# Optimization experiments

Measured on AMD Instinct MI355X. Metric: run time of the kernel, lower is better.

Reference implementation:

```python
import jax, jax.numpy as jnp
import numpy as np

B, T, D, H = 4, 3072, 1024, 16
HD = D // H

def setup_inputs() -> dict:
    key = jax.random.key(0)
    ks = jax.random.split(key, 7)
    s = 1.0 / np.sqrt(D)
    x = jax.random.normal(ks[0], (B, T, D), dtype=jnp.float32)
    Wq = jax.random.normal(ks[1], (D, D), dtype=jnp.float32) * s
    Wk = jax.random.normal(ks[2], (D, D), dtype=jnp.float32) * s
    Wv = jax.random.normal(ks[3], (D, D), dtype=jnp.float32) * s
    Wo = jax.random.normal(ks[4], (D, D), dtype=jnp.float32) * s
    bo = jnp.zeros((D,), dtype=jnp.float32)
    Wconv = jax.random.normal(ks[5], (D, D, 3), dtype=jnp.float32) * (1.0 / np.sqrt(3 * D))  # (out, in, kw)
    return {"x": x, "Wq": Wq, "Wk": Wk, "Wv": Wv, "Wo": Wo, "bo": bo, "Wconv": Wconv}

def reference(x, Wq, Wk, Wv, Wo, bo, Wconv):
    b, t, d = x.shape
    # stride-3 conv pooling of K/V stream (Conv1d(D, D, 3, stride=3, bias=False))
    kc = jax.lax.conv_general_dilated(
        x.transpose(0, 2, 1), Wconv, window_strides=(3,), padding='VALID',
        dimension_numbers=('NCH', 'OIH', 'NCH')).transpose(0, 2, 1)  # (B, T//3, D)
    k_tmp = jnp.concatenate([x[:, :1, :], kc], axis=1)  # (B, Tk, D)
    tk = k_tmp.shape[1]
    # comparison-based bias mask: masked where 3*k_idx >= q_idx + 0.001
    q_idx = jnp.arange(t, dtype=jnp.float32)
    k_idx = jnp.arange(tk, dtype=jnp.float32)
    mask = (k_idx[None, :] * 3.0 >= q_idx[:, None] + 0.001).astype(x.dtype)  # (T, Tk)
    # projections (torch Linear: y = x @ W.T)
    q = x @ Wq.T
    k = k_tmp @ Wk.T
    v = k_tmp @ Wv.T
    q = q.reshape(b, t, H, HD).transpose(0, 2, 1, 3)   # (B, H, T, HD)
    k = k.reshape(b, tk, H, HD).transpose(0, 2, 1, 3)  # (B, H, Tk, HD)
    v = v.reshape(b, tk, H, HD).transpose(0, 2, 1, 3)
    scores = jnp.einsum('bhqd,bhkd->bhqk', q, k) * (HD ** -0.5)
    scores = scores + mask * jnp.asarray(-1e9, dtype=x.dtype)
    p = jax.nn.softmax(scores, axis=-1)  # dropout is identity in eval (p=0)
    o = jnp.einsum('bhqk,bhkd->bhqd', p, v)
    o = o.transpose(0, 2, 1, 3).reshape(b, t, d)
    return o @ Wo.T + bo
```

## Files before the change

### kernel.cpp

```cpp
#include <hip/hip_runtime.h>
#include <hip/hip_bf16.h>
#include <cstdint>
#include <cstddef>

typedef __attribute__((ext_vector_type(8))) __bf16 bf16x8;
typedef __attribute__((ext_vector_type(4))) __bf16 bf16x4;
typedef __attribute__((ext_vector_type(4))) float  floatx4;

#define MFMA16x16x32(a, b, c) __builtin_amdgcn_mfma_f32_16x16x32_bf16((a), (b), (c), 0, 0, 0)

#define ATTN_SC 0.18033688011112042f

__device__ __forceinline__ void gload_lds16(const void* g, void* l) {
  __builtin_amdgcn_global_load_lds((const __attribute__((address_space(1))) void*)g,
                                   (__attribute__((address_space(3))) void*)l,
                                   16, 0, 0);
}


__global__ void prep_kernel(const float* __restrict__ x,
                            const float* __restrict__ Wq, const float* __restrict__ Wk,
                            const float* __restrict__ Wv, const float* __restrict__ Wo,
                            const float* __restrict__ Wconv,
                            __bf16* __restrict__ xb,
                            __bf16* __restrict__ wqb, __bf16* __restrict__ wkb,
                            __bf16* __restrict__ wvb, __bf16* __restrict__ wob,
                            __bf16* __restrict__ wc2, __bf16* __restrict__ ktmp) {
  const int bid = blockIdx.x, tid = threadIdx.x;
  if (bid < 4096) {
    const int which = bid >> 10;
    const float* src = (which == 0) ? Wq : (which == 1) ? Wk : (which == 2) ? Wv : Wo;
    __bf16* dst = (which == 0) ? wqb : (which == 1) ? wkb : (which == 2) ? wvb : wob;
    const int i = (bid & 1023) * 256 + tid;
    floatx4 v = *(const floatx4*)(src + (size_t)i * 4);
    bf16x4 o; o[0] = (__bf16)v[0]; o[1] = (__bf16)v[1]; o[2] = (__bf16)v[2]; o[3] = (__bf16)v[3];
    *(bf16x4*)(dst + (size_t)i * 4) = o;
  } else if (bid < 5120) {
    const int t = (bid - 4096) * 256 + tid;
    const int o = t >> 8, c = t & 255;
    const float* base = Wconv + (size_t)o * 3072 + c * 12;
    float f[12];
    *(floatx4*)(f)     = *(const floatx4*)(base);
    *(floatx4*)(f + 4) = *(const floatx4*)(base + 4);
    *(floatx4*)(f + 8) = *(const floatx4*)(base + 8);
#pragma unroll
    for (int kw = 0; kw < 3; ++kw) {
      bf16x4 q;
#pragma unroll
      for (int j = 0; j < 4; ++j) q[j] = (__bf16)f[3 * j + kw];
      *(bf16x4*)(wc2 + (size_t)o * 3072 + kw * 1024 + c * 4) = q;
    }
  } else if (bid < 5136) {
    const int i = (bid - 5120) * 256 + tid;
    const int b = i >> 10, c = i & 1023;
    ktmp[(size_t)b * 1025 * 1024 + c] = (__bf16)x[(size_t)b * 3072 * 1024 + c];
  } else {
    const int i = (bid - 5136) * 256 + tid;
    floatx4 v = *(const floatx4*)(x + (size_t)i * 4);
    bf16x4 o; o[0] = (__bf16)v[0]; o[1] = (__bf16)v[1]; o[2] = (__bf16)v[2]; o[3] = (__bf16)v[3];
    *(bf16x4*)(xb + (size_t)i * 4) = o;
  }
}

__global__ void vtrans_kernel(const __bf16* __restrict__ V, __bf16* __restrict__ Vt) {
  __shared__ __attribute__((aligned(16))) __bf16 tile[64][72];
  const int tid = threadIdx.x;
  const int bh = blockIdx.y;
  const int b = bh >> 4, h = bh & 15;
  const int t0 = blockIdx.x * 64;
  const int r = tid >> 3, s = tid & 7;
#pragma unroll
  for (int p = 0; p < 2; ++p) {
    const int t = p * 32 + r;
    bf16x8 v = *(const bf16x8*)(V + ((size_t)(b * 1025 + t0 + t)) * 1024 + h * 64 + s * 8);
    *(bf16x8*)(&tile[t][s * 8]) = v;
  }
  __syncthreads();
#pragma unroll
  for (int p = 0; p < 2; ++p) {
    const int d = p * 32 + r;
    bf16x8 o;
#pragma unroll
    for (int e = 0; e < 8; ++e) o[e] = tile[s * 8 + e][d];
    *(bf16x8*)(Vt + ((size_t)bh * 64 + d) * 1024 + t0 + s * 8) = o;
  }
}


template <int MODE>
__device__ __forceinline__ void gemm8_body(
    const __bf16* __restrict__ A, const __bf16* __restrict__ Bw, void* __restrict__ Cout,
    const float* __restrict__ bias, int N, int K, int m0, int n0,
    __bf16* As, __bf16* Bs)
{
  const int tid  = threadIdx.x;
  const int wave = tid >> 6;
  const int lane = tid & 63;
  const int g    = lane >> 4;
  const int ln   = lane & 15;
  const int wr   = (wave >> 2) * 64;
  const int wc   = (wave & 3) * 64;

  const int prow = tid >> 3;
  const int pc   = tid & 7;
  const int ca   = pc ^ (prow & 7);
  const size_t aSrc  = (size_t)(m0 + prow + ((ca >> 2) << 6)) * K + ((ca & 3) << 3);
  const size_t bSrc0 = (size_t)(n0 + prow + ((ca >> 2) << 7)) * K + ((ca & 3) << 3);
  const size_t bSrc1 = bSrc0 + (size_t)64 * K;

  int aOff[4], bOff[4];
#pragma unroll
  for (int i = 0; i < 4; ++i) {
    const int ra = wr + i * 16 + ln;
    const int pr = ra & 63;
    const int c  = ((ra >> 6) << 2) + g;
    aOff[i] = pr * 64 + ((c ^ (pr & 7)) << 3);
  }
#pragma unroll
  for (int j = 0; j < 4; ++j) {
    const int rb = wc + j * 16 + ln;
    const int pr = rb & 127;
    const int c  = ((rb >> 7) << 2) + g;
    bOff[j] = pr * 64 + ((c ^ (pr & 7)) << 3);
  }

  floatx4 acc[4][4];
#pragma unroll
  for (int i = 0; i < 4; ++i)
#pragma unroll
    for (int j = 0; j < 4; ++j) { floatx4 z = {0.f, 0.f, 0.f, 0.f}; acc[i][j] = z; }

  __bf16* const ad0 = As + (tid << 3);
  __bf16* const bd0 = Bs + (tid << 3);

  auto STAGE = [&](int halfidx) {
    const int slot = halfidx & 3;
    const int koff = (halfidx >> 1) * 64 + ((halfidx & 1) << 5);
    gload_lds16(A  + aSrc  + koff, ad0 + (slot << 12));
    gload_lds16(Bw + bSrc0 + koff, bd0 + (slot << 13));
    gload_lds16(Bw + bSrc1 + koff, bd0 + (slot << 13) + 4096);
  };

  bf16x8 afA[4], bfA[4], afB[4], bfB[4];

#define READF(AF, BF, slot)                                                        \
  {                                                                                \
    const __bf16* ah_ = As + ((slot) << 12);                                       \
    const __bf16* bh_ = Bs + ((slot) << 13);                                       \
    _Pragma("unroll")                                                              \
    for (int i_ = 0; i_ < 4; ++i_) AF[i_] = *(const bf16x8*)(ah_ + aOff[i_]);      \
    _Pragma("unroll")                                                              \
    for (int j_ = 0; j_ < 4; ++j_) BF[j_] = *(const bf16x8*)(bh_ + bOff[j_]);      \
  }

#define MFMAC(AF, BF)                                                              \
  {                                                                                \
    __builtin_amdgcn_s_setprio(1);                                                 \
    _Pragma("unroll")                                                              \
    for (int i_ = 0; i_ < 4; ++i_)                                                 \
      _Pragma("unroll")                                                            \
      for (int j_ = 0; j_ < 4; ++j_)                                               \
        acc[i_][j_] = MFMA16x16x32(AF[i_], BF[j_], acc[i_][j_]);                   \
    __builtin_amdgcn_s_setprio(0);                                                 \
  }

#define PHASE_WAIT(x)                                                              \
  {                                                                                \
    if ((x) + 4 < HT)      { asm volatile("s_waitcnt vmcnt(6) lgkmcnt(0)" ::: "memory"); } \
    else if ((x) + 3 < HT) { asm volatile("s_waitcnt vmcnt(3) lgkmcnt(0)" ::: "memory"); } \
    else                   { asm volatile("s_waitcnt vmcnt(0) lgkmcnt(0)" ::: "memory"); } \
  }

  const int HT = K >> 5;

  STAGE(0); STAGE(1); STAGE(2);
  asm volatile("s_waitcnt vmcnt(6)" ::: "memory");
  __builtin_amdgcn_s_barrier();
  __builtin_amdgcn_sched_barrier(0);
  READF(afA, bfA, 0);
  STAGE(3);
  asm volatile("s_waitcnt vmcnt(6) lgkmcnt(0)" ::: "memory");

  for (int h = 0; h < HT; h += 2) {
    __builtin_amdgcn_s_barrier();
    __builtin_amdgcn_sched_barrier(0);
    READF(afB, bfB, (h + 1) & 3);
    MFMAC(afA, bfA);
    if (h + 4 < HT) STAGE(h + 4);
    PHASE_WAIT(h);

    __builtin_amdgcn_s_barrier();
    __builtin_amdgcn_sched_barrier(0);
    if (h + 2 < HT) READF(afA, bfA, (h + 2) & 3);
    MFMAC(afB, bfB);
    if (h + 2 < HT) {
      if (h + 5 < HT) STAGE(h + 5);
      PHASE_WAIT(h + 1);
    }
  }

#undef READF
#undef MFMAC
#undef PHASE_WAIT

#pragma unroll
  for (int j = 0; j < 4; ++j) {
    const int col = n0 + wc + j * 16 + ln;
    float bj = 0.f;
    if (MODE == 2) bj = bias[col];
#pragma unroll
    for (int i = 0; i < 4; ++i)
#pragma unroll
      for (int r = 0; r < 4; ++r) {
        const int row = m0 + wr + i * 16 + g * 4 + r;
        if (MODE == 2) {
          ((float*)Cout)[(size_t)row * N + col] = acc[i][j][r] + bj;
        } else if (MODE == 1) {
          const size_t orow = (size_t)(row >> 10) * 1025 + 1 + (row & 1023);
          ((__bf16*)Cout)[orow * 1024 + col] = (__bf16)acc[i][j][r];
        } else if (MODE == 4) {
          ((__bf16*)Cout)[(size_t)row * N + col] = (__bf16)(acc[i][j][r] * ATTN_SC);
        } else {
          ((__bf16*)Cout)[(size_t)row * N + col] = (__bf16)acc[i][j][r];
        }
      }
  }
}

__global__ __launch_bounds__(512, 2) void gemm_convq_kernel(
    const __bf16* __restrict__ xb, const __bf16* __restrict__ wc2,
    const __bf16* __restrict__ wqb, __bf16* __restrict__ ktmp, __bf16* __restrict__ qb)
{
  __shared__ __attribute__((aligned(16))) __bf16 As[16384];
  __shared__ __attribute__((aligned(16))) __bf16 Bs[32768];
  const int xcd = blockIdx.x & 7, s = blockIdx.x >> 3;
  if (s < 16) {
    const int id = xcd * 16 + s;
    gemm8_body<1>(xb, wc2, ktmp, nullptr, 1024, 3072, (id >> 2) * 128, (id & 3) * 256, As, Bs);
  } else {
    const int id = xcd * 48 + (s - 16);
    gemm8_body<4>(xb, wqb, qb, nullptr, 1024, 1024, (id >> 2) * 128, (id & 3) * 256, As, Bs);
  }
}

__global__ __launch_bounds__(512, 2) void gemm_kv_kernel(
    const __bf16* __restrict__ ktmp, const __bf16* __restrict__ wkb,
    const __bf16* __restrict__ wvb, __bf16* __restrict__ kb, __bf16* __restrict__ vb)
{
  __shared__ __attribute__((aligned(16))) __bf16 As[16384];
  __shared__ __attribute__((aligned(16))) __bf16 Bs[32768];
  const int id = (blockIdx.x & 7) * 33 + (blockIdx.x >> 3);
  const int p  = (id >= 132) ? 1 : 0;
  const int rest = id - p * 132;
  gemm8_body<0>(ktmp, p ? wvb : wkb, p ? vb : kb, nullptr, 1024, 1024,
                (rest >> 2) * 128, (rest & 3) * 256, As, Bs);
}

__global__ __launch_bounds__(512, 2) void gemm_o_kernel(
    const __bf16* __restrict__ ob, const __bf16* __restrict__ wob,
    float* __restrict__ out, const float* __restrict__ bo)
{
  __shared__ __attribute__((aligned(16))) __bf16 As[16384];
  __shared__ __attribute__((aligned(16))) __bf16 Bs[32768];
  const int id = (blockIdx.x & 7) * 48 + (blockIdx.x >> 3);
  gemm8_body<2>(ob, wob, out, bo, 1024, 1024, (id >> 2) * 128, (id & 3) * 256, As, Bs);
}


__global__ __launch_bounds__(256) void attn_kernel(
    const __bf16* __restrict__ Q, const __bf16* __restrict__ Kk,
    const __bf16* __restrict__ Vt, __bf16* __restrict__ O)
{
  __shared__ __attribute__((aligned(16))) __bf16 Kd[2][64 * 64];
  __shared__ __attribute__((aligned(16))) __bf16 Vd[2][64 * 64];
  __shared__ __attribute__((aligned(16))) __bf16 Ps[4][32 * 64];

  const int tid  = threadIdx.x;
  const int wave = tid >> 6;
  const int lane = tid & 63;
  const int g    = lane >> 4;
  const int ln   = lane & 15;

  const int l    = blockIdx.x;
  const int xcd  = l & 7;
  const int b    = xcd >> 1;
  const int rest = l >> 3;
  const int h    = rest & 15;
  const int qt   = ((11 - (rest >> 4)) << 1) | (xcd & 1);
  const int q0   = qt * 128 + wave * 32;

  const size_t qrow0 = (size_t)b * 3072 + q0;
  const size_t krow0 = (size_t)b * 1025;
  const size_t vtrow = ((size_t)(b * 16 + h)) * 64;
  const int hc = h * 64;
  const int sw = (ln & 7) << 3;
  __bf16* Pw = Ps[wave];

  const int srow = lane >> 3;
  const int scol = (lane & 7) * 8;

  auto stage = [&](int kt, int bb) {
    const int kb0 = kt * 64;
#pragma unroll
    for (int i = 0; i < 2; ++i) {
      const int rr = (wave * 2 + i) * 8 + srow;
      gload_lds16(Kk + (krow0 + kb0 + rr) * 1024 + hc + scol,
                  Kd[bb] + (size_t)rr * 64 + scol);
      gload_lds16(Vt + (vtrow + rr) * 1024 + kb0 + scol,
                  Vd[bb] + (size_t)rr * 64 + scol);
    }
  };

  bf16x8 qf[2][2];
#pragma unroll
  for (int i = 0; i < 2; ++i)
#pragma unroll
    for (int kc = 0; kc < 2; ++kc)
      qf[i][kc] = *(const bf16x8*)(Q + (qrow0 + i * 16 + ln) * 1024 + hc + kc * 32 + g * 8);

  floatx4 oacc[2][4];
  floatx4 oal[2];
#pragma unroll
  for (int i = 0; i < 2; ++i) {
    floatx4 z = {0.f, 0.f, 0.f, 0.f};
    oal[i] = z;
#pragma unroll
    for (int dt = 0; dt < 4; ++dt) oacc[i][dt] = z;
  }

  bf16x8 ones;
#pragma unroll
  for (int e = 0; e < 8; ++e) ones[e] = (__bf16)1.0f;

  const int nkt_blk = (((qt * 128 + 127) / 3) >> 6) + 1;
  const int nfull   = (q0 >= 189) ? ((q0 - 189) / 192 + 1) : 0;

  stage(0, 0);

  for (int kt = 0; kt < nkt_blk; ++kt) {
    const int bb = kt & 1;
    __syncthreads();
    if (kt + 1 < nkt_blk) stage(kt + 1, bb ^ 1);
    const int kb0 = kt * 64;
    const bool masked = (kt >= nfull);

    bf16x8 kf[4][2];
#pragma unroll
    for (int jk = 0; jk < 4; ++jk)
#pragma unroll
      for (int kc = 0; kc < 2; ++kc)
        kf[jk][kc] = *(const bf16x8*)(Kd[bb] + (jk * 16 + ln) * 64 + kc * 32 + g * 8);

#pragma unroll
    for (int jk = 0; jk < 4; ++jk)
#pragma unroll
      for (int i = 0; i < 2; ++i) {
        floatx4 s = {0.f, 0.f, 0.f, 0.f};
        s = MFMA16x16x32(kf[jk][0], qf[i][0], s);
        s = MFMA16x16x32(kf[jk][1], qf[i][1], s);
        float p[4];
#pragma unroll
        for (int r = 0; r < 4; ++r) {
          float e = __builtin_amdgcn_exp2f(s[r]);
          if (masked) {
            const int key = kb0 + jk * 16 + 4 * g + r;
            const int q   = q0 + i * 16 + ln;
            e = (3 * key <= q) ? e : 0.f;
          }
          p[r] = e;
        }
        bf16x4 pk;
        pk[0] = (__bf16)p[0]; pk[1] = (__bf16)p[1]; pk[2] = (__bf16)p[2]; pk[3] = (__bf16)p[3];
        *(bf16x4*)(Pw + (i * 16 + ln) * 64 + ((jk * 16 + 4 * g) ^ sw)) = pk;
      }

#pragma unroll
    for (int kc = 0; kc < 2; ++kc) {
      bf16x8 pf0 = *(const bf16x8*)(Pw + (ln) * 64      + ((kc * 32 + g * 8) ^ sw));
      bf16x8 pf1 = *(const bf16x8*)(Pw + (16 + ln) * 64 + ((kc * 32 + g * 8) ^ sw));
      oal[0] = MFMA16x16x32(ones, pf0, oal[0]);
      oal[1] = MFMA16x16x32(ones, pf1, oal[1]);
#pragma unroll
      for (int dt = 0; dt < 4; ++dt) {
        bf16x8 vf = *(const bf16x8*)(Vd[bb] + (dt * 16 + ln) * 64 + kc * 32 + g * 8);
        oacc[0][dt] = MFMA16x16x32(vf, pf0, oacc[0][dt]);
        oacc[1][dt] = MFMA16x16x32(vf, pf1, oacc[1][dt]);
      }
    }
  }

#pragma unroll
  for (int i = 0; i < 2; ++i) {
    const float inv = 1.0f / oal[i][0];
    const size_t row = qrow0 + i * 16 + ln;
#pragma unroll
    for (int dt = 0; dt < 4; ++dt) {
      bf16x4 o4;
#pragma unroll
      for (int r = 0; r < 4; ++r) o4[r] = (__bf16)(oacc[i][dt][r] * inv);
      *(bf16x4*)(O + row * 1024 + hc + dt * 16 + 4 * g) = o4;
    }
  }
}


extern "C" void kernel_launch(void* const* d_in, const int* in_sizes, int n_in,
                              void* d_out, int out_size, void* d_ws, size_t ws_size,
                              hipStream_t stream) {
  (void)in_sizes; (void)n_in; (void)out_size; (void)ws_size;
  const float* x     = (const float*)d_in[0];
  const float* Wq    = (const float*)d_in[1];
  const float* Wk    = (const float*)d_in[2];
  const float* Wv    = (const float*)d_in[3];
  const float* Wo    = (const float*)d_in[4];
  const float* bo    = (const float*)d_in[5];
  const float* Wconv = (const float*)d_in[6];

  char* ws = (char*)d_ws;
  const size_t SZ_XQ = (size_t)12288 * 1024 * 2;
  const size_t SZ_KT = (size_t)4224 * 1024 * 2;
  const size_t SZ_W  = (size_t)1024 * 1024 * 2;

  __bf16* xb   = (__bf16*)(ws);
  __bf16* qb   = (__bf16*)(ws + SZ_XQ);
  __bf16* ktmp = (__bf16*)(ws + 2 * SZ_XQ);
  __bf16* kb   = (__bf16*)(ws + 2 * SZ_XQ + SZ_KT);
  __bf16* vb   = (__bf16*)(ws + 2 * SZ_XQ + 2 * SZ_KT);
  __bf16* wqb  = (__bf16*)(ws + 2 * SZ_XQ + 3 * SZ_KT);
  __bf16* wkb  = (__bf16*)(ws + 2 * SZ_XQ + 3 * SZ_KT + SZ_W);
  __bf16* wvb  = (__bf16*)(ws + 2 * SZ_XQ + 3 * SZ_KT + 2 * SZ_W);
  __bf16* wob  = (__bf16*)(ws + 2 * SZ_XQ + 3 * SZ_KT + 3 * SZ_W);
  __bf16* wc2  = (__bf16*)(ws + 2 * SZ_XQ + 3 * SZ_KT + 4 * SZ_W);
  __bf16* vt   = xb;

  prep_kernel<<<dim3(17424), dim3(256), 0, stream>>>(x, Wq, Wk, Wv, Wo, Wconv,
                                                     xb, wqb, wkb, wvb, wob, wc2, ktmp);
  gemm_convq_kernel<<<dim3(512), dim3(512), 0, stream>>>(xb, wc2, wqb, ktmp, qb);
  gemm_kv_kernel<<<dim3(264), dim3(512), 0, stream>>>(ktmp, wkb, wvb, kb, vb);
  vtrans_kernel<<<dim3(16, 64), dim3(256), 0, stream>>>(vb, vt);
  attn_kernel<<<dim3(1536), dim3(256), 0, stream>>>(qb, kb, vt, qb);
  gemm_o_kernel<<<dim3(384), dim3(512), 0, stream>>>(qb, wob, (float*)d_out, bo);
}
```

Measured before the change: 344.8 us.

## Restructure GEMM mainloop into 3-stage full-tile LDS ring with one barrier per tile

The shared GEMM body replaces its 4-slot ring of half-K (32) tiles, which needed two barriers per 64-wide K step, with a 3-stage ring of full 64-wide K tiles. Each step prefetches two tiles ahead and needs only one barrier and one wait. The aim is to cut barrier and waitcnt overhead and deepen prefetch for the projection GEMMs. In exchange, LDS per block grows from 96KB to 144KB. Both K halves are now read from LDS before any MFMA is issued, which may reduce overlap between LDS reads and MFMAs and raise register pressure.

```diff
diff --git a/kernel.cpp b/kernel.cpp
--- a/kernel.cpp
+++ b/kernel.cpp
@@ -133,20 +133,24 @@
   __bf16* const ad0 = As + (tid << 3);
   __bf16* const bd0 = Bs + (tid << 3);
 
-  auto STAGE = [&](int halfidx) {
-    const int slot = halfidx & 3;
-    const int koff = (halfidx >> 1) * 64 + ((halfidx & 1) << 5);
-    gload_lds16(A  + aSrc  + koff, ad0 + (slot << 12));
-    gload_lds16(Bw + bSrc0 + koff, bd0 + (slot << 13));
-    gload_lds16(Bw + bSrc1 + koff, bd0 + (slot << 13) + 4096);
+  auto STAGE = [&](int t, int p) {
+    const int koff = t * 64;
+    __bf16* a0 = ad0 + (2 * p) * 4096;
+    __bf16* b0 = bd0 + (2 * p) * 8192;
+    gload_lds16(A  + aSrc  + koff,      a0);
+    gload_lds16(Bw + bSrc0 + koff,      b0);
+    gload_lds16(Bw + bSrc1 + koff,      b0 + 4096);
+    gload_lds16(A  + aSrc  + koff + 32, a0 + 4096);
+    gload_lds16(Bw + bSrc0 + koff + 32, b0 + 8192);
+    gload_lds16(Bw + bSrc1 + koff + 32, b0 + 12288);
   };
 
-  bf16x8 afA[4], bfA[4], afB[4], bfB[4];
-
-#define READF(AF, BF, slot)                                                        \
+  bf16x8 af0[4], bf0[4], af1[4], bf1[4];
+
+#define READF(AF, BF, s)                                                           \
   {                                                                                \
-    const __bf16* ah_ = As + ((slot) << 12);                                       \
-    const __bf16* bh_ = Bs + ((slot) << 13);                                       \
+    const __bf16* ah_ = As + (s) * 4096;                                           \
+    const __bf16* bh_ = Bs + (s) * 8192;                                           \
     _Pragma("unroll")                                                              \
     for (int i_ = 0; i_ < 4; ++i_) AF[i_] = *(const bf16x8*)(ah_ + aOff[i_]);      \
     _Pragma("unroll")                                                              \
@@ -164,44 +168,36 @@
     __builtin_amdgcn_s_setprio(0);                                                 \
   }
 
-#define PHASE_WAIT(x)                                                              \
-  {                                                                                \
-    if ((x) + 4 < HT)      { asm volatile("s_waitcnt vmcnt(6) lgkmcnt(0)" ::: "memory"); } \
-    else if ((x) + 3 < HT) { asm volatile("s_waitcnt vmcnt(3) lgkmcnt(0)" ::: "memory"); } \
-    else                   { asm volatile("s_waitcnt vmcnt(0) lgkmcnt(0)" ::: "memory"); } \
-  }
-
-  const int HT = K >> 5;
-
-  STAGE(0); STAGE(1); STAGE(2);
+  const int NT = K >> 6;
+
+  STAGE(0, 0);
+  STAGE(1, 1);
   asm volatile("s_waitcnt vmcnt(6)" ::: "memory");
   __builtin_amdgcn_s_barrier();
   __builtin_amdgcn_sched_barrier(0);
-  READF(afA, bfA, 0);
-  STAGE(3);
-  asm volatile("s_waitcnt vmcnt(6) lgkmcnt(0)" ::: "memory");
-
-  for (int h = 0; h < HT; h += 2) {
-    __builtin_amdgcn_s_barrier();
-    __builtin_amdgcn_sched_barrier(0);
-    READF(afB, bfB, (h + 1) & 3);
-    MFMAC(afA, bfA);
-    if (h + 4 < HT) STAGE(h + 4);
-    PHASE_WAIT(h);
-
-    __builtin_amdgcn_s_barrier();
-    __builtin_amdgcn_sched_barrier(0);
-    if (h + 2 < HT) READF(afA, bfA, (h + 2) & 3);
-    MFMAC(afB, bfB);
-    if (h + 2 < HT) {
-      if (h + 5 < HT) STAGE(h + 5);
-      PHASE_WAIT(h + 1);
-    }
+
+  int p = 0;
+  for (int t = 0; t < NT; ++t) {
+    const int pn = (p + 2 >= 3) ? p - 1 : p + 2;
+    if (t + 2 < NT) STAGE(t + 2, pn);
+    READF(af0, bf0, 2 * p);
+    READF(af1, bf1, 2 * p + 1);
+    MFMAC(af0, bf0);
+    MFMAC(af1, bf1);
+    if (t + 2 < NT) {
+      asm volatile("s_waitcnt vmcnt(6) lgkmcnt(0)" ::: "memory");
+    } else if (t + 1 < NT) {
+      asm volatile("s_waitcnt vmcnt(0) lgkmcnt(0)" ::: "memory");
+    }
+    if (t + 1 < NT) {
+      __builtin_amdgcn_s_barrier();
+      __builtin_amdgcn_sched_barrier(0);
+    }
+    p = (p + 1 >= 3) ? 0 : p + 1;
   }
 
 #undef READF
 #undef MFMAC
-#undef PHASE_WAIT
 
 #pragma unroll
   for (int j = 0; j < 4; ++j) {
@@ -231,8 +227,8 @@
     const __bf16* __restrict__ xb, const __bf16* __restrict__ wc2,
     const __bf16* __restrict__ wqb, __bf16* __restrict__ ktmp, __bf16* __restrict__ qb)
 {
-  __shared__ __attribute__((aligned(16))) __bf16 As[16384];
-  __shared__ __attribute__((aligned(16))) __bf16 Bs[32768];
+  __shared__ __attribute__((aligned(16))) __bf16 As[24576];
+  __shared__ __attribute__((aligned(16))) __bf16 Bs[49152];
   const int xcd = blockIdx.x & 7, s = blockIdx.x >> 3;
   if (s < 16) {
     const int id = xcd * 16 + s;
@@ -247,8 +243,8 @@
     const __bf16* __restrict__ ktmp, const __bf16* __restrict__ wkb,
     const __bf16* __restrict__ wvb, __bf16* __restrict__ kb, __bf16* __restrict__ vb)
 {
-  __shared__ __attribute__((aligned(16))) __bf16 As[16384];
-  __shared__ __attribute__((aligned(16))) __bf16 Bs[32768];
+  __shared__ __attribute__((aligned(16))) __bf16 As[24576];
+  __shared__ __attribute__((aligned(16))) __bf16 Bs[49152];
   const int id = (blockIdx.x & 7) * 33 + (blockIdx.x >> 3);
   const int p  = (id >= 132) ? 1 : 0;
   const int rest = id - p * 132;
@@ -260,8 +256,8 @@
     const __bf16* __restrict__ ob, const __bf16* __restrict__ wob,
     float* __restrict__ out, const float* __restrict__ bo)
 {
-  __shared__ __attribute__((aligned(16))) __bf16 As[16384];
-  __shared__ __attribute__((aligned(16))) __bf16 Bs[32768];
+  __shared__ __attribute__((aligned(16))) __bf16 As[24576];
+  __shared__ __attribute__((aligned(16))) __bf16 Bs[49152];
   const int id = (blockIdx.x & 7) * 48 + (blockIdx.x >> 3);
   gemm8_body<2>(ob, wob, out, bo, 1024, 1024, (id >> 2) * 128, (id & 3) * 256, As, Bs);
 }
```

Measured after the change: 359.8 us. +4.3%, slower.
